# Kernel optimization log

Hardware: AMD Instinct MI355X
Metric: run time of the kernel (lower is better)

## Reference

```python
import jax, jax.numpy as jnp
import numpy as np

B, C, IMG, P, E, H, F, L, NC = 32, 1, 224, 16, 256, 16, 3072, 12, 8
NP_ = (IMG // P) ** 2          # 196 patches
S = NP_ + 1                    # 197 tokens (cls + patches)
HD = E // H                    # 16 head dim
DVL, DVR, DVT = NP_ // 4 + 1, NP_ // 4, NP_ // 4   # 50, 49, 49 -> sum + DVT = 197


def _ln(x, g, b, eps=1e-5):
    m = x.mean(-1, keepdims=True)
    v = ((x - m) ** 2).mean(-1, keepdims=True)
    return (x - m) / jnp.sqrt(v + eps) * g + b


def setup_inputs():
    key = jax.random.key(0)
    ks = iter(jax.random.split(key, 64))
    def w(shape, s=0.02):
        return jax.random.normal(next(ks), shape, jnp.float32) * s
    return dict(
        x=jax.random.normal(next(ks), (B, C, IMG, IMG), jnp.float32),
        W_patch=w((E, C, P, P)), b_patch=jnp.zeros((E,), jnp.float32),
        cls_tok=w((1, 1, E), 1.0), pos_emb=w((1, S, E), 1.0),
        Wkl=w((E, E)), bkl=jnp.zeros((E,), jnp.float32),
        Wvl=w((DVL, E)), bvl=jnp.zeros((DVL,), jnp.float32),
        Wkr=w((E, E)), bkr=jnp.zeros((E,), jnp.float32),
        Wvr=w((DVR, E)), bvr=jnp.zeros((DVR,), jnp.float32),
        Wkt=w((E, E)), bkt=jnp.zeros((E,), jnp.float32),
        Wvt=w((DVT, E)), bvt=jnp.zeros((DVT,), jnp.float32),
        ln1_g=jnp.ones((L, E), jnp.float32), ln1_b=jnp.zeros((L, E), jnp.float32),
        Wqkv=w((L, 3 * E, E)), bqkv=jnp.zeros((L, 3 * E), jnp.float32),
        Wo=w((L, E, E)), bo=jnp.zeros((L, E), jnp.float32),
        ln2_g=jnp.ones((L, E), jnp.float32), ln2_b=jnp.zeros((L, E), jnp.float32),
        W1=w((L, F, E)), b1=jnp.zeros((L, F), jnp.float32),
        W2=w((L, E, F)), b2=jnp.zeros((L, E), jnp.float32),
        lnf_g=jnp.ones((E,), jnp.float32), lnf_b=jnp.zeros((E,), jnp.float32),
        W_head=w((NC, E)), b_head=jnp.zeros((NC,), jnp.float32),
    )


def reference(x, W_patch, b_patch, cls_tok, pos_emb,
              Wkl, bkl, Wvl, bvl, Wkr, bkr, Wvr, bvr, Wkt, bkt, Wvt, bvt,
              ln1_g, ln1_b, Wqkv, bqkv, Wo, bo, ln2_g, ln2_b, W1, b1, W2, b2,
              lnf_g, lnf_b, W_head, b_head):
    Bsz = x.shape[0]
    scale_k = 1.0 / jnp.sqrt(jnp.float32(E))
    # patch embedding: conv with stride == kernel == patch size
    h = jax.lax.conv_general_dilated(x, W_patch, (P, P), 'VALID',
                                     dimension_numbers=('NCHW', 'OIHW', 'NCHW'))
    h = h + b_patch[None, :, None, None]                   # (B, E, 14, 14)
    h = h.reshape(Bsz, E, NP_).transpose(0, 2, 1)          # (B, 196, E)
    h = jnp.concatenate([jnp.broadcast_to(cls_tok, (Bsz, 1, E)), h], 1) + pos_emb

    # linear rotatory attention fusing each sample with its batch neighbors
    def rag(xl, xt, xr):                                   # each (S, E)
        rt = xt.mean(0)                                    # target summary (E,)
        al = jax.nn.softmax((xl @ Wkl.T + bkl) @ rt * scale_k)
        rl = al @ (xl @ Wvl.T + bvl)                       # (DVL,)
        ar = jax.nn.softmax((xr @ Wkr.T + bkr) @ rt * scale_k)
        rr = ar @ (xr @ Wvr.T + bvr)                       # (DVR,)
        kt = xt @ Wkt.T + bkt
        vt = xt @ Wvt.T + bvt
        rtl = jax.nn.softmax(kt @ xl.mean(0) * scale_k) @ vt   # (DVT,)
        rtr = jax.nn.softmax(kt @ xr.mean(0) * scale_k) @ vt   # (DVT,)
        f = jnp.concatenate([rl, rtl, rtr, rr])            # (S,) = 50+49+49+49
        return jnp.outer(f, rt)                            # (S, E)

    mid = jax.vmap(rag)(h[:-2], h[1:-1], h[2:])            # (B-2, S, E) batched (no per-sample loop)
    h = jnp.concatenate([h[:1], mid, h[-1:]], 0)

    # standard pre-LN transformer encoder, scanned over stacked layer params
    def block(carry, p):
        g1, b1n, wqkv, bq, wo, bo_, g2, b2n, w1, bb1, w2, bb2 = p
        xn = _ln(carry, g1, b1n)
        qkv = xn @ wqkv.T + bq                             # (B, S, 3E)
        q, k, v = jnp.split(qkv, 3, axis=-1)
        q = q.reshape(Bsz, S, H, HD)
        k = k.reshape(Bsz, S, H, HD)
        v = v.reshape(Bsz, S, H, HD)
        att = jnp.einsum('bqhd,bkhd->bhqk', q, k) / jnp.sqrt(jnp.float32(HD))
        att = jax.nn.softmax(att, axis=-1)
        o = jnp.einsum('bhqk,bkhd->bqhd', att, v).reshape(Bsz, S, E)
        carry = carry + o @ wo.T + bo_
        xn2 = _ln(carry, g2, b2n)
        ff = jax.nn.gelu(xn2 @ w1.T + bb1, approximate=False) @ w2.T + bb2
        return carry + ff, None

    h, _ = jax.lax.scan(block, h, (ln1_g, ln1_b, Wqkv, bqkv, Wo, bo,
                                   ln2_g, ln2_b, W1, b1, W2, b2))
    cls = _ln(h[:, 0], lnf_g, lnf_b)
    return cls @ W_head.T + b_head
```

## Files before the change

kernel.cpp:

```cpp
#include <hip/hip_runtime.h>
#include <hip/hip_bf16.h>
#include <math.h>

constexpr int Bz  = 32;
constexpr int S   = 197;
constexpr int E   = 256;
constexpr int Hn  = 16;
constexpr int HD  = 16;
constexpr int Fd  = 3072;
constexpr int Ln  = 12;
constexpr int MS  = Bz * S;
constexpr int MP  = 6400;
constexpr int NPAT = 6272;
constexpr int DVL = 50, DVR = 49, DVT = 49;
constexpr size_t WLSTRIDE = 1835008;

typedef __attribute__((ext_vector_type(8))) short short8;
typedef __attribute__((ext_vector_type(4))) short short4v;
typedef __attribute__((ext_vector_type(4))) float f32x4;

__device__ __forceinline__ unsigned short f2bf(float f) {
    unsigned int u = __float_as_uint(f);
    u = (u + 0x7FFFu + ((u >> 16) & 1u)) >> 16;
    return (unsigned short)u;
}

__device__ __forceinline__ void gload_lds16(const void* g, void* l) {
    __builtin_amdgcn_global_load_lds(
        (const __attribute__((address_space(1))) void*)g,
        (__attribute__((address_space(3))) void*)l, 16, 0, 0);
}

__device__ __forceinline__ float wave_reduce(float v, int op) {
    #pragma unroll
    for (int off = 32; off > 0; off >>= 1) {
        float o = __shfl_xor(v, off, 64);
        v = op ? fmaxf(v, o) : v + o;
    }
    return v;
}

__device__ __forceinline__ float block_reduce(float v, float* red4, int op) {
    v = wave_reduce(v, op);
    int w = threadIdx.x >> 6;
    if ((threadIdx.x & 63) == 0) red4[w] = v;
    __syncthreads();
    float r = op ? fmaxf(fmaxf(red4[0], red4[1]), fmaxf(red4[2], red4[3]))
                 : (red4[0] + red4[1] + red4[2] + red4[3]);
    __syncthreads();
    return r;
}

__device__ __forceinline__ float gelu_f(float v) {
    return 0.5f * v * (1.f + erff(v * 0.70710678118654752f));
}

__global__ __launch_bounds__(256) void patchify_kernel(
        const float* __restrict__ x, unsigned short* __restrict__ Ab) {
    int pi = blockIdx.x;
    int b = pi / 196, q = pi % 196;
    int i = q / 14, j = q % 14;
    int e = threadIdx.x, pr = e >> 4, pc = e & 15;
    float v = x[((size_t)(b * 224 + i * 16 + pr)) * 224 + j * 16 + pc];
    Ab[(size_t)pi * 256 + e] = f2bf(v);
}

__global__ __launch_bounds__(256) void cls_pos_kernel(
        const float* __restrict__ cls, const float* __restrict__ pos,
        float* __restrict__ h0) {
    int b = blockIdx.x, e = threadIdx.x;
    h0[(size_t)(b * S) * E + e] = cls[e] + pos[e];
}

__global__ __launch_bounds__(256) void convert_kernel(
        const float* __restrict__ src, unsigned short* __restrict__ dst) {
    int i4 = (blockIdx.x * 256 + threadIdx.x) * 4;
    float4 v = *(const float4*)(src + i4);
    ushort4 o;
    o.x = f2bf(v.x); o.y = f2bf(v.y); o.z = f2bf(v.z); o.w = f2bf(v.w);
    *(ushort4*)(dst + i4) = o;
}

__global__ __launch_bounds__(256) void convert_w_all_kernel(
        const float* __restrict__ wqkv, const float* __restrict__ wo,
        const float* __restrict__ w1, const float* __restrict__ w2,
        unsigned short* __restrict__ out) {
    size_t idx = (size_t)blockIdx.x * 256 + threadIdx.x;
    int l = (int)(idx / 458752);
    int r4 = (int)(idx % 458752) * 4;
    const float* src;
    if (r4 < 196608)       src = wqkv + (size_t)l * 196608 + r4;
    else if (r4 < 262144)  src = wo   + (size_t)l * 65536  + (r4 - 196608);
    else if (r4 < 1048576) src = w1   + (size_t)l * 786432 + (r4 - 262144);
    else                   src = w2   + (size_t)l * 786432 + (r4 - 1048576);
    float4 v = *(const float4*)src;
    ushort4 o;
    o.x = f2bf(v.x); o.y = f2bf(v.y); o.z = f2bf(v.z); o.w = f2bf(v.w);
    *(ushort4*)(out + (size_t)l * WLSTRIDE + r4) = o;
}

__global__ __launch_bounds__(256) void means_kernel(
        const float* __restrict__ h0, float* __restrict__ M) {
    __shared__ float part[4][256];
    int b = blockIdx.x, tid = threadIdx.x, w = tid >> 6, lane = tid & 63;
    float4 a = {0.f, 0.f, 0.f, 0.f};
    for (int t = w; t < S; t += 4) {
        float4 v = *(const float4*)&h0[((size_t)(b * S + t)) * E + lane * 4];
        a.x += v.x; a.y += v.y; a.z += v.z; a.w += v.w;
    }
    *(float4*)&part[w][lane * 4] = a;
    __syncthreads();
    M[b * E + tid] = (part[0][tid] + part[1][tid] + part[2][tid] + part[3][tid])
                     * (1.f / (float)S);
}

__global__ __launch_bounds__(256) void uvec_kernel(
        const float* __restrict__ M,
        const float* __restrict__ Wkl, const float* __restrict__ bkl,
        const float* __restrict__ Wkr, const float* __restrict__ bkr,
        const float* __restrict__ Wkt, const float* __restrict__ bkt,
        float* __restrict__ Ul, float* __restrict__ Ur, float* __restrict__ Ut,
        float* __restrict__ cl, float* __restrict__ cr, float* __restrict__ ct) {
    __shared__ float p0[4][256], p1[4][256], p2[4][256], red4[4];
    int t = blockIdx.x, tid = threadIdx.x, w = tid >> 6, lane = tid & 63;
    const float* mt = M + t * E;
    float4 a0 = {0,0,0,0}, a1 = {0,0,0,0}, a2 = {0,0,0,0};
    for (int i = w * 64; i < w * 64 + 64; i++) {
        float mi = mt[i];
        float4 v0 = *(const float4*)&Wkl[(size_t)i * 256 + lane * 4];
        float4 v1 = *(const float4*)&Wkr[(size_t)i * 256 + lane * 4];
        float4 v2 = *(const float4*)&Wkt[(size_t)i * 256 + lane * 4];
        a0.x += v0.x * mi; a0.y += v0.y * mi; a0.z += v0.z * mi; a0.w += v0.w * mi;
        a1.x += v1.x * mi; a1.y += v1.y * mi; a1.z += v1.z * mi; a1.w += v1.w * mi;
        a2.x += v2.x * mi; a2.y += v2.y * mi; a2.z += v2.z * mi; a2.w += v2.w * mi;
    }
    *(float4*)&p0[w][lane * 4] = a0;
    *(float4*)&p1[w][lane * 4] = a1;
    *(float4*)&p2[w][lane * 4] = a2;
    __syncthreads();
    Ul[t * E + tid] = p0[0][tid] + p0[1][tid] + p0[2][tid] + p0[3][tid];
    Ur[t * E + tid] = p1[0][tid] + p1[1][tid] + p1[2][tid] + p1[3][tid];
    Ut[t * E + tid] = p2[0][tid] + p2[1][tid] + p2[2][tid] + p2[3][tid];
    float me = mt[tid];
    float c0 = block_reduce(bkl[tid] * me, red4, 0);
    float c1 = block_reduce(bkr[tid] * me, red4, 0);
    float c2 = block_reduce(bkt[tid] * me, red4, 0);
    if (tid == 0) { cl[t] = c0; cr[t] = c1; ct[t] = c2; }
}

__global__ __launch_bounds__(256) void rag_score_kernel(
        const float* __restrict__ h0, const float* __restrict__ M,
        const float* __restrict__ Ul, const float* __restrict__ Ur,
        const float* __restrict__ Ut,
        const float* __restrict__ cl, const float* __restrict__ cr,
        const float* __restrict__ ct,
        const float* __restrict__ Wvl, const float* __restrict__ bvl,
        const float* __restrict__ Wvr, const float* __restrict__ bvr,
        const float* __restrict__ Wvt, const float* __restrict__ bvt,
        float* __restrict__ fbuf) {
    int t = blockIdx.x >> 2, br = blockIdx.x & 3;
    const float* xsrc; const float* u; float c;
    const float* Wv; const float* bv; int dv, fo;
    if (br == 0)      { xsrc = h0 + (size_t)t * S * E;       u = Ul + (t+1)*E; c = cl[t+1]; Wv = Wvl; bv = bvl; dv = DVL; fo = 0; }
    else if (br == 1) { xsrc = h0 + (size_t)(t+1) * S * E;   u = Ut + t*E;     c = ct[t];   Wv = Wvt; bv = bvt; dv = DVT; fo = DVL; }
    else if (br == 2) { xsrc = h0 + (size_t)(t+1) * S * E;   u = Ut + (t+2)*E; c = ct[t+2]; Wv = Wvt; bv = bvt; dv = DVT; fo = DVL + DVT; }
    else              { xsrc = h0 + (size_t)(t+2) * S * E;   u = Ur + (t+1)*E; c = cr[t+1]; Wv = Wvr; bv = bvr; dv = DVR; fo = DVL + 2*DVT; }
    __shared__ float us[256], sc[200], xbar[256], part[4][256], red4[4];
    int tid = threadIdx.x, w = tid >> 6, lane = tid & 63;
    us[tid] = u[tid];
    __syncthreads();
    float4 u4 = *(float4*)&us[lane * 4];
    for (int s = w; s < S; s += 4) {
        float4 x4 = *(const float4*)&xsrc[(size_t)s * E + lane * 4];
        float p = x4.x*u4.x + x4.y*u4.y + x4.z*u4.z + x4.w*u4.w;
        p = wave_reduce(p, 0);
        if (lane == 0) sc[s] = (p + c) * 0.0625f;
    }
    __syncthreads();
    float v = (tid < S) ? sc[tid] : -1e30f;
    float mx = block_reduce(v, red4, 1);
    float ex = (tid < S) ? expf(v - mx) : 0.f;
    float dn = block_reduce(ex, red4, 0);
    if (tid < S) sc[tid] = ex / dn;
    __syncthreads();
    float4 pa = {0.f, 0.f, 0.f, 0.f};
    for (int s = w; s < S; s += 4) {
        float a = sc[s];
        float4 x4 = *(const float4*)&xsrc[(size_t)s * E + lane * 4];
        pa.x += a * x4.x; pa.y += a * x4.y; pa.z += a * x4.z; pa.w += a * x4.w;
    }
    *(float4*)&part[w][lane * 4] = pa;
    __syncthreads();
    xbar[tid] = part[0][tid] + part[1][tid] + part[2][tid] + part[3][tid];
    __syncthreads();
    float4 xb4 = *(float4*)&xbar[lane * 4];
    for (int d = w; d < dv; d += 4) {
        float4 w4 = *(const float4*)&Wv[(size_t)d * E + lane * 4];
        float p = w4.x*xb4.x + w4.y*xb4.y + w4.z*xb4.z + w4.w*xb4.w;
        p = wave_reduce(p, 0);
        if (lane == 0) fbuf[t * 256 + fo + d] = p + bv[d];
    }
}

__global__ __launch_bounds__(256) void rag_outer_kernel(
        const float* __restrict__ fbuf, const float* __restrict__ M,
        float* __restrict__ h1) {
    int bid = blockIdx.x;
    int t = bid / S, s = bid % S;
    float f = fbuf[t * 256 + s];
    int e = threadIdx.x;
    h1[((size_t)((t + 1) * S + s)) * E + e] = f * M[(t + 1) * E + e];
}

__global__ __launch_bounds__(256) void copy_edges(const float* __restrict__ h0,
                                                  float* __restrict__ h1) {
    int i = blockIdx.x * 256 + threadIdx.x;
    int n = S * E;
    if (i < n) h1[i] = h0[i];
    else if (i < 2 * n) {
        int j = i - n;
        size_t o = (size_t)31 * S * E + j;
        h1[o] = h0[o];
    }
}

__global__ __launch_bounds__(256) void ln_kernel(const float* __restrict__ in,
                                                 unsigned short* __restrict__ out,
                                                 const float* __restrict__ g,
                                                 const float* __restrict__ b) {
    int w = threadIdx.x >> 6, lane = threadIdx.x & 63;
    int tok = blockIdx.x * 4 + w;
    const float* row = in + (size_t)tok * E;
    float4 v = *(const float4*)&row[lane * 4];
    float mean = wave_reduce(v.x + v.y + v.z + v.w, 0) * (1.f / 256.f);
    float dx = v.x - mean, dy = v.y - mean, dz = v.z - mean, dw = v.w - mean;
    float var = wave_reduce(dx*dx + dy*dy + dz*dz + dw*dw, 0) * (1.f / 256.f);
    float inv = rsqrtf(var + 1e-5f);
    float4 gg = *(const float4*)&g[lane * 4];
    float4 bb = *(const float4*)&b[lane * 4];
    ushort4 o;
    o.x = f2bf(dx * inv * gg.x + bb.x);
    o.y = f2bf(dy * inv * gg.y + bb.y);
    o.z = f2bf(dz * inv * gg.z + bb.z);
    o.w = f2bf(dw * inv * gg.w + bb.w);
    *(ushort4*)&out[(size_t)tok * E + lane * 4] = o;
}

template <int MODE>
__global__ __launch_bounds__(256) void gemm_s64(
        const unsigned short* __restrict__ A, int lda,
        const unsigned short* __restrict__ W, int ldw,
        const float* __restrict__ bias,
        void* __restrict__ Cv, int ldc, int K, int MT, int NT,
        const float* __restrict__ pos) {
    constexpr bool SWAP = (MODE == 4);
    __shared__ unsigned short As[2 * 64 * 64];
    __shared__ unsigned short Bs[2 * 64 * 64];
    const int id = blockIdx.x;
    const int mt = (id & 7) + 8 * (id / (8 * NT));
    const int nt = (id >> 3) % NT;
    if (mt >= MT) return;
    const int m0 = mt * 64, n0 = nt * 64;
    const int tid = threadIdx.x, wave = tid >> 6, lane = tid & 63;
    const int lr = lane & 15, kg = lane >> 4;
    const int srow = wave * 16 + (lane >> 3);
    const int scol = ((lane & 7) ^ (lane >> 3)) * 8;
    auto stage = [&](int bb, int k0) {
        #pragma unroll
        for (int q = 0; q < 2; q++) {
            gload_lds16(&A[(size_t)(m0 + srow + q * 8) * lda + k0 + scol],
                        &As[bb * 4096 + (wave * 16 + q * 8) * 64]);
            gload_lds16(&W[(size_t)(n0 + srow + q * 8) * ldw + k0 + scol],
                        &Bs[bb * 4096 + (wave * 16 + q * 8) * 64]);
        }
    };
    const int nIter = K >> 6;
    stage(0, 0);
    f32x4 acc[4] = {};
    for (int i = 0; i < nIter; i++) {
        __syncthreads();
        if (i + 1 < nIter) stage((i + 1) & 1, (i + 1) * 64);
        const int bb = i & 1;
        #pragma unroll
        for (int h = 0; h < 2; h++) {
            const int sw = ((h * 4 + kg) ^ (lr & 7)) * 8;
            short8 af = *(short8*)&As[bb * 4096 + (wave * 16 + lr) * 64 + sw];
            #pragma unroll
            for (int j = 0; j < 4; j++) {
                short8 bf = *(short8*)&Bs[bb * 4096 + (j * 16 + lr) * 64 + sw];
                if (SWAP)
                    acc[j] = __builtin_amdgcn_mfma_f32_16x16x32_bf16(bf, af, acc[j], 0, 0, 0);
                else
                    acc[j] = __builtin_amdgcn_mfma_f32_16x16x32_bf16(af, bf, acc[j], 0, 0, 0);
            }
        }
    }
    if (SWAP) {
        __syncthreads();
        unsigned short* T = As + wave * 1152;
        #pragma unroll
        for (int j = 0; j < 4; j++) {
            int nb = n0 + j * 16 + kg * 4;
            float4 b4 = *(const float4*)&bias[nb];
            ushort4 pk;
            pk.x = f2bf(acc[j][0] + b4.x);
            pk.y = f2bf(acc[j][1] + b4.y);
            pk.z = f2bf(acc[j][2] + b4.z);
            pk.w = f2bf(acc[j][3] + b4.w);
            *(ushort4*)&T[lr * 72 + j * 16 + kg * 4] = pk;
        }
        int rrow = lane >> 3, cg = (lane & 7) * 8;
        #pragma unroll
        for (int g = 0; g < 2; g++) {
            int row = g * 8 + rrow;
            short8 val = *(short8*)&T[row * 72 + cg];
            int m = m0 + wave * 16 + row;
            *(short8*)&((unsigned short*)Cv)[(size_t)m * ldc + n0 + cg] = val;
        }
    } else {
        #pragma unroll
        for (int j = 0; j < 4; j++) {
            int n = n0 + j * 16 + lr;
            float bv = bias ? bias[n] : 0.f;
            #pragma unroll
            for (int r = 0; r < 4; r++) {
                int m = m0 + wave * 16 + kg * 4 + r;
                float v = acc[j][r] + bv;
                if (MODE == 1) ((float*)Cv)[(size_t)m * ldc + n] += v;
                if (MODE == 3) {
                    int b = m / 196, s = m - b * 196 + 1;
                    ((float*)Cv)[((size_t)(b * S + s)) * E + n] = v + pos[(size_t)s * E + n];
                }
            }
        }
    }
}

template <int MODE>
__global__ __launch_bounds__(256) void gemm_s128(
        const unsigned short* __restrict__ A, int lda,
        const unsigned short* __restrict__ W, int ldw,
        const float* __restrict__ bias,
        void* __restrict__ Cv, int ldc, int K, int MT, int NT) {
    __shared__ unsigned short As[2 * 128 * 64];
    __shared__ unsigned short Bs[2 * 128 * 64];
    const int id = blockIdx.x;
    const int mt = (id & 7) + 8 * (id / (8 * NT));
    const int nt = (id >> 3) % NT;
    if (mt >= MT) return;
    const int m0 = mt * 128, n0 = nt * 128;
    const int tid = threadIdx.x, wave = tid >> 6, lane = tid & 63;
    const int wm = (wave >> 1) * 64, wn = (wave & 1) * 64;
    const int lr = lane & 15, kg = lane >> 4;
    const int srow = wave * 32 + (lane >> 3);
    const int scol = ((lane & 7) ^ (lane >> 3)) * 8;
    auto stage = [&](int bb, int k0) {
        #pragma unroll
        for (int q = 0; q < 4; q++) {
            gload_lds16(&A[(size_t)(m0 + srow + q * 8) * lda + k0 + scol],
                        &As[bb * 8192 + (wave * 4 + q) * 512]);
            gload_lds16(&W[(size_t)(n0 + srow + q * 8) * ldw + k0 + scol],
                        &Bs[bb * 8192 + (wave * 4 + q) * 512]);
        }
    };
    const int nIter = K >> 6;
    stage(0, 0);
    f32x4 acc[4][4] = {};
    for (int i = 0; i < nIter; i++) {
        __syncthreads();
        if (i + 1 < nIter) stage((i + 1) & 1, (i + 1) * 64);
        const int bb = i & 1;
        #pragma unroll
        for (int h = 0; h < 2; h++) {
            const int sw = ((h * 4 + kg) ^ (lr & 7)) * 8;
            short8 af[4], bfr[4];
            #pragma unroll
            for (int i2 = 0; i2 < 4; i2++) af[i2]  = *(short8*)&As[bb * 8192 + (wm + i2 * 16 + lr) * 64 + sw];
            #pragma unroll
            for (int j = 0; j < 4; j++) bfr[j] = *(short8*)&Bs[bb * 8192 + (wn + j * 16 + lr) * 64 + sw];
            #pragma unroll
            for (int i2 = 0; i2 < 4; i2++)
                #pragma unroll
                for (int j = 0; j < 4; j++)
                    acc[i2][j] = __builtin_amdgcn_mfma_f32_16x16x32_bf16(bfr[j], af[i2], acc[i2][j], 0, 0, 0);
        }
    }
    __syncthreads();
    unsigned short* T = As + wave * 2304;
    #pragma unroll
    for (int half = 0; half < 2; half++) {
        #pragma unroll
        for (int ii = 0; ii < 2; ii++) {
            int i = half * 2 + ii;
            #pragma unroll
            for (int j = 0; j < 4; j++) {
                int nb = n0 + wn + j * 16 + kg * 4;
                float4 b4 = *(const float4*)&bias[nb];
                ushort4 pk;
                pk.x = f2bf(gelu_f(acc[i][j][0] + b4.x));
                pk.y = f2bf(gelu_f(acc[i][j][1] + b4.y));
                pk.z = f2bf(gelu_f(acc[i][j][2] + b4.z));
                pk.w = f2bf(gelu_f(acc[i][j][3] + b4.w));
                *(ushort4*)&T[(ii * 16 + lr) * 72 + j * 16 + kg * 4] = pk;
            }
        }
        int rrow = lane >> 3, cg = (lane & 7) * 8;
        #pragma unroll
        for (int g = 0; g < 4; g++) {
            int row = g * 8 + rrow;
            short8 val = *(short8*)&T[row * 72 + cg];
            int m = m0 + wm + half * 32 + row;
            *(short8*)&((unsigned short*)Cv)[(size_t)m * ldc + n0 + wn + cg] = val;
        }
        if (half == 0) __syncthreads();
    }
}

static inline int sg(int MT, int NT) { return ((MT + 7) / 8) * 8 * NT; }

__global__ __launch_bounds__(256) void attn_kernel(
        const unsigned short* __restrict__ qkv, unsigned short* __restrict__ o) {
    int b = blockIdx.x >> 4, hh = blockIdx.x & 15;
    __shared__ unsigned short Qs[208][32];
    __shared__ unsigned short Ks[208][32];
    __shared__ unsigned short Vt[16][224];
    __shared__ unsigned short Ps[4][16][224];
    int tid = threadIdx.x, wave = tid >> 6, lane = tid & 63;
    int lr = lane & 15, kg = lane >> 4;
    short8 z8 = {};
    if (tid < 208) {
        if (tid < 197) {
            size_t row = (size_t)(b * S + tid) * 768 + hh * 16;
            *(short8*)&Qs[tid][0] = *(const short8*)&qkv[row];
            *(short8*)&Qs[tid][8] = *(const short8*)&qkv[row + 8];
            *(short8*)&Ks[tid][0] = *(const short8*)&qkv[row + 256];
            *(short8*)&Ks[tid][8] = *(const short8*)&qkv[row + 264];
            union { short8 v8[2]; unsigned short u[16]; } vv;
            vv.v8[0] = *(const short8*)&qkv[row + 512];
            vv.v8[1] = *(const short8*)&qkv[row + 520];
            #pragma unroll
            for (int d = 0; d < 16; d++) Vt[d][tid] = vv.u[d];
        } else {
            *(short8*)&Qs[tid][0] = z8; *(short8*)&Qs[tid][8] = z8;
            *(short8*)&Ks[tid][0] = z8; *(short8*)&Ks[tid][8] = z8;
            #pragma unroll
            for (int d = 0; d < 16; d++) Vt[d][tid] = 0;
        }
        *(short8*)&Qs[tid][16] = z8; *(short8*)&Qs[tid][24] = z8;
        *(short8*)&Ks[tid][16] = z8; *(short8*)&Ks[tid][24] = z8;
    } else if (tid < 224) {
        #pragma unroll
        for (int d = 0; d < 16; d++) Vt[d][tid] = 0;
    }
    {
        short4v z4 = {};
        *(short4v*)&Ps[wave][lane >> 2][208 + (lane & 3) * 4] = z4;
    }
    __syncthreads();
    const f32x4 zf = {0.f, 0.f, 0.f, 0.f};
    for (int it = wave; it < 13; it += 4) {
        short8 qa = *(short8*)&Qs[it * 16 + lr][kg * 8];
        f32x4 sc[13];
        #pragma unroll
        for (int j = 0; j < 13; j++) {
            short8 kb = *(short8*)&Ks[j * 16 + lr][kg * 8];
            sc[j] = __builtin_amdgcn_mfma_f32_16x16x32_bf16(qa, kb, zf, 0, 0, 0);
        }
        float m[4] = {-1e30f, -1e30f, -1e30f, -1e30f};
        #pragma unroll
        for (int j = 0; j < 13; j++) {
            if (j * 16 + lr < 197) {
                #pragma unroll
                for (int r = 0; r < 4; r++) m[r] = fmaxf(m[r], sc[j][r]);
            }
        }
        #pragma unroll
        for (int off = 1; off < 16; off <<= 1)
            #pragma unroll
            for (int r = 0; r < 4; r++) m[r] = fmaxf(m[r], __shfl_xor(m[r], off, 64));
        float l[4] = {0.f, 0.f, 0.f, 0.f};
        #pragma unroll
        for (int j = 0; j < 13; j++) {
            bool valid = (j * 16 + lr) < 197;
            #pragma unroll
            for (int r = 0; r < 4; r++) {
                float p = valid ? __expf((sc[j][r] - m[r]) * 0.25f) : 0.f;
                l[r] += p;
                Ps[wave][kg * 4 + r][j * 16 + lr] = f2bf(p);
            }
        }
        #pragma unroll
        for (int off = 1; off < 16; off <<= 1)
            #pragma unroll
            for (int r = 0; r < 4; r++) l[r] += __shfl_xor(l[r], off, 64);
        f32x4 oa = zf;
        #pragma unroll
        for (int k0 = 0; k0 < 224; k0 += 32) {
            short8 pa = *(short8*)&Ps[wave][lr][k0 + kg * 8];
            short8 vb = *(short8*)&Vt[lr][k0 + kg * 8];
            oa = __builtin_amdgcn_mfma_f32_16x16x32_bf16(pa, vb, oa, 0, 0, 0);
        }
        #pragma unroll
        for (int r = 0; r < 4; r++) {
            int q = it * 16 + kg * 4 + r;
            if (q < 197)
                o[((size_t)(b * S + q)) * 256 + hh * 16 + lr] = f2bf(oa[r] / l[r]);
        }
    }
}

__global__ __launch_bounds__(256) void head_kernel(
        const float* __restrict__ h, const float* __restrict__ g,
        const float* __restrict__ bb, const float* __restrict__ Wh,
        const float* __restrict__ bh, float* __restrict__ out) {
    __shared__ float red4[4];
    __shared__ float xs[256];
    int b = blockIdx.x, e = threadIdx.x;
    float v = h[((size_t)(b * S)) * E + e];
    float mean = block_reduce(v, red4, 0) * (1.f / 256.f);
    float d = v - mean;
    float var = block_reduce(d * d, red4, 0) * (1.f / 256.f);
    float xn = d * rsqrtf(var + 1e-5f) * g[e] + bb[e];
    xs[e] = xn;
    __syncthreads();
    for (int n = 0; n < 8; n++) {
        float s = block_reduce(xs[e] * Wh[(size_t)n * 256 + e], red4, 0);
        if (e == 0) out[b * 8 + n] = s + bh[n];
    }
}

extern "C" void kernel_launch(void* const* d_in, const int* in_sizes, int n_in,
                              void* d_out, int out_size, void* d_ws, size_t ws_size,
                              hipStream_t stream) {
    const float* x      = (const float*)d_in[0];
    const float* W_patch= (const float*)d_in[1];
    const float* b_patch= (const float*)d_in[2];
    const float* cls_tok= (const float*)d_in[3];
    const float* pos_emb= (const float*)d_in[4];
    const float* Wkl = (const float*)d_in[5];   const float* bkl = (const float*)d_in[6];
    const float* Wvl = (const float*)d_in[7];   const float* bvl = (const float*)d_in[8];
    const float* Wkr = (const float*)d_in[9];   const float* bkr = (const float*)d_in[10];
    const float* Wvr = (const float*)d_in[11];  const float* bvr = (const float*)d_in[12];
    const float* Wkt = (const float*)d_in[13];  const float* bkt = (const float*)d_in[14];
    const float* Wvt = (const float*)d_in[15];  const float* bvt = (const float*)d_in[16];
    const float* ln1_g = (const float*)d_in[17]; const float* ln1_b = (const float*)d_in[18];
    const float* Wqkv  = (const float*)d_in[19]; const float* bqkv  = (const float*)d_in[20];
    const float* Wo    = (const float*)d_in[21]; const float* bo    = (const float*)d_in[22];
    const float* ln2_g = (const float*)d_in[23]; const float* ln2_b = (const float*)d_in[24];
    const float* W1 = (const float*)d_in[25];   const float* b1 = (const float*)d_in[26];
    const float* W2 = (const float*)d_in[27];   const float* b2 = (const float*)d_in[28];
    const float* lnf_g = (const float*)d_in[29]; const float* lnf_b = (const float*)d_in[30];
    const float* W_head = (const float*)d_in[31]; const float* b_head = (const float*)d_in[32];

    char* p = (char*)d_ws;
    float* h0 = (float*)p;                    p += (size_t)MP * 256 * 4;
    float* h1 = (float*)p;                    p += (size_t)MP * 256 * 4;
    unsigned short* qkb = (unsigned short*)p; p += (size_t)MP * 768 * 2;
    unsigned short* xnb = (unsigned short*)p; p += (size_t)MP * 256 * 2;
    unsigned short* ob  = (unsigned short*)p; p += (size_t)MP * 256 * 2;
    unsigned short* ff  = (unsigned short*)p; p += (size_t)MP * 3072 * 2;
    unsigned short* wpb = (unsigned short*)p; p += (size_t)65536 * 2;
    float* ragws = (float*)p;                 p += (size_t)40960 * 4;
    unsigned short* wall = (unsigned short*)p;
    float* M    = ragws;
    float* Ul   = ragws + 8192;
    float* Ur   = ragws + 2 * 8192;
    float* Ut   = ragws + 3 * 8192;
    float* cl   = ragws + 4 * 8192;
    float* cr   = cl + 32;
    float* ct   = cl + 64;
    float* fbuf = cl + 96;

    convert_w_all_kernel<<<21504, 256, 0, stream>>>(Wqkv, Wo, W1, W2, wall);

    convert_kernel<<<64, 256, 0, stream>>>(W_patch, wpb);
    patchify_kernel<<<NPAT, 256, 0, stream>>>(x, xnb);
    cls_pos_kernel<<<Bz, 256, 0, stream>>>(cls_tok, pos_emb, h0);
    gemm_s64<3><<<sg(98, 4), 256, 0, stream>>>(
        xnb, 256, wpb, 256, b_patch, h0, 256, 256, 98, 4, pos_emb);

    means_kernel<<<Bz, 256, 0, stream>>>(h0, M);
    uvec_kernel<<<Bz, 256, 0, stream>>>(M, Wkl, bkl, Wkr, bkr, Wkt, bkt,
                                        Ul, Ur, Ut, cl, cr, ct);
    rag_score_kernel<<<(Bz - 2) * 4, 256, 0, stream>>>(
        h0, M, Ul, Ur, Ut, cl, cr, ct, Wvl, bvl, Wvr, bvr, Wvt, bvt, fbuf);
    rag_outer_kernel<<<(Bz - 2) * S, 256, 0, stream>>>(fbuf, M, h1);
    copy_edges<<<(2 * S * E + 255) / 256, 256, 0, stream>>>(h0, h1);

    for (int l = 0; l < Ln; l++) {
        const unsigned short* wqkv_b = wall + (size_t)l * WLSTRIDE;
        const unsigned short* wo_b   = wqkv_b + 196608;
        const unsigned short* w1_b   = wqkv_b + 262144;
        const unsigned short* w2_b   = wqkv_b + 1048576;
        ln_kernel<<<MS / 4, 256, 0, stream>>>(h1, xnb, ln1_g + l * E, ln1_b + l * E);
        gemm_s64<4><<<sg(100, 12), 256, 0, stream>>>(
            xnb, 256, wqkv_b, 256, bqkv + l * 768, qkb, 768, 256, 100, 12, nullptr);
        attn_kernel<<<Bz * Hn, 256, 0, stream>>>(qkb, ob);
        gemm_s64<1><<<sg(100, 4), 256, 0, stream>>>(
            ob, 256, wo_b, 256, bo + l * 256, h1, 256, 256, 100, 4, nullptr);
        ln_kernel<<<MS / 4, 256, 0, stream>>>(h1, xnb, ln2_g + l * E, ln2_b + l * E);
        gemm_s128<2><<<sg(50, 24), 256, 0, stream>>>(
            xnb, 256, w1_b, 256, b1 + l * Fd, ff, 3072, 256, 50, 24);
        gemm_s64<1><<<sg(100, 4), 256, 0, stream>>>(
            ff, 3072, w2_b, 3072, b2 + l * 256, h1, 256, 3072, 100, 4, nullptr);
    }
    head_kernel<<<Bz, 256, 0, stream>>>(h1, lnf_g, lnf_b, W_head, b_head, (float*)d_out);
}
```

Baseline: 1.637 ms.

## Specialize FFN1 GEMM: preload full A tile, stream W from global, polynomial GELU

The FFN1 GEMM becomes a specialized kernel with K fixed at 256. It loads the whole 128x256 A tile into LDS once with a single barrier, and streams weight fragments straight from global memory into registers, double-buffered across the eight k-steps. This removes the per-iteration barriers and the LDS staging for B. It also replaces erff in GELU with the Abramowitz-Stegun polynomial plus __expf, which cuts epilogue cost but adds an approximation error of about 1e-7 in erf.

Result: slower. 1.772 ms (+8.3%).

```diff
diff --git a/kernel.cpp b/kernel.cpp
--- a/kernel.cpp
+++ b/kernel.cpp
@@ -52,7 +52,14 @@
 }
 
 __device__ __forceinline__ float gelu_f(float v) {
-    return 0.5f * v * (1.f + erff(v * 0.70710678118654752f));
+    float x  = v * 0.70710678118654752f;
+    float ax = fabsf(x);
+    float t  = 1.0f / fmaf(0.3275911f, ax, 1.0f);
+    float p  = t * fmaf(t, fmaf(t, fmaf(t, fmaf(t, 1.061405429f, -1.453152027f),
+                                        1.421413741f), -0.284496736f), 0.254829592f);
+    float er = 1.0f - p * __expf(-x * x);
+    er = copysignf(er, x);
+    return 0.5f * v * (1.0f + er);
 }
 
 __global__ __launch_bounds__(256) void patchify_kernel(
@@ -336,14 +343,14 @@
     }
 }
 
-template <int MODE>
-__global__ __launch_bounds__(256) void gemm_s128(
-        const unsigned short* __restrict__ A, int lda,
-        const unsigned short* __restrict__ W, int ldw,
+__global__ __launch_bounds__(256) void gemm_ffn1(
+        const unsigned short* __restrict__ A,
+        const unsigned short* __restrict__ W,
         const float* __restrict__ bias,
-        void* __restrict__ Cv, int ldc, int K, int MT, int NT) {
-    __shared__ unsigned short As[2 * 128 * 64];
-    __shared__ unsigned short Bs[2 * 128 * 64];
+        unsigned short* __restrict__ Cv,
+        int MT, int NT) {
+    constexpr int LDA = 256, LDW = 256, LDC = 3072;
+    __shared__ unsigned short As[4 * 128 * 64];
     const int id = blockIdx.x;
     const int mt = (id & 7) + 8 * (id / (8 * NT));
     const int nt = (id >> 3) % NT;
@@ -354,35 +361,39 @@
     const int lr = lane & 15, kg = lane >> 4;
     const int srow = wave * 32 + (lane >> 3);
     const int scol = ((lane & 7) ^ (lane >> 3)) * 8;
-    auto stage = [&](int bb, int k0) {
-        #pragma unroll
-        for (int q = 0; q < 4; q++) {
-            gload_lds16(&A[(size_t)(m0 + srow + q * 8) * lda + k0 + scol],
-                        &As[bb * 8192 + (wave * 4 + q) * 512]);
-            gload_lds16(&W[(size_t)(n0 + srow + q * 8) * ldw + k0 + scol],
-                        &Bs[bb * 8192 + (wave * 4 + q) * 512]);
-        }
+    #pragma unroll
+    for (int c = 0; c < 4; c++)
+        #pragma unroll
+        for (int q = 0; q < 4; q++)
+            gload_lds16(&A[(size_t)(m0 + srow + q * 8) * LDA + c * 64 + scol],
+                        &As[c * 8192 + (wave * 4 + q) * 512]);
+    const unsigned short* Wrow[4];
+    #pragma unroll
+    for (int j = 0; j < 4; j++)
+        Wrow[j] = W + (size_t)(n0 + wn + j * 16 + lr) * LDW + kg * 8;
+    f32x4 acc[4][4] = {};
+    short8 bfA[4], bfB[4];
+    auto loadB = [&](short8 (&dst)[4], int s) {
+        #pragma unroll
+        for (int j = 0; j < 4; j++)
+            dst[j] = *(const short8*)(Wrow[j] + s * 32);
     };
-    const int nIter = K >> 6;
-    stage(0, 0);
-    f32x4 acc[4][4] = {};
-    for (int i = 0; i < nIter; i++) {
-        __syncthreads();
-        if (i + 1 < nIter) stage((i + 1) & 1, (i + 1) * 64);
-        const int bb = i & 1;
-        #pragma unroll
-        for (int h = 0; h < 2; h++) {
-            const int sw = ((h * 4 + kg) ^ (lr & 7)) * 8;
-            short8 af[4], bfr[4];
-            #pragma unroll
-            for (int i2 = 0; i2 < 4; i2++) af[i2]  = *(short8*)&As[bb * 8192 + (wm + i2 * 16 + lr) * 64 + sw];
-            #pragma unroll
-            for (int j = 0; j < 4; j++) bfr[j] = *(short8*)&Bs[bb * 8192 + (wn + j * 16 + lr) * 64 + sw];
-            #pragma unroll
-            for (int i2 = 0; i2 < 4; i2++)
-                #pragma unroll
-                for (int j = 0; j < 4; j++)
-                    acc[i2][j] = __builtin_amdgcn_mfma_f32_16x16x32_bf16(bfr[j], af[i2], acc[i2][j], 0, 0, 0);
+    loadB(bfA, 0);
+    __syncthreads();
+    #pragma unroll
+    for (int s = 0; s < 8; s++) {
+        const int c = s >> 1, h = s & 1;
+        const int sw = ((h * 4 + kg) ^ (lr & 7)) * 8;
+        short8 (&cur)[4] = (s & 1) ? bfB : bfA;
+        short8 (&nxt)[4] = (s & 1) ? bfA : bfB;
+        if (s < 7) loadB(nxt, s + 1);
+        #pragma unroll
+        for (int i2 = 0; i2 < 4; i2++) {
+            short8 af = *(short8*)&As[c * 8192 + (wm + i2 * 16 + lr) * 64 + sw];
+            #pragma unroll
+            for (int j = 0; j < 4; j++)
+                acc[i2][j] = __builtin_amdgcn_mfma_f32_16x16x32_bf16(
+                        cur[j], af, acc[i2][j], 0, 0, 0);
         }
     }
     __syncthreads();
@@ -410,7 +421,7 @@
             int row = g * 8 + rrow;
             short8 val = *(short8*)&T[row * 72 + cg];
             int m = m0 + wm + half * 32 + row;
-            *(short8*)&((unsigned short*)Cv)[(size_t)m * ldc + n0 + wn + cg] = val;
+            *(short8*)&Cv[(size_t)m * LDC + n0 + wn + cg] = val;
         }
         if (half == 0) __syncthreads();
     }
@@ -599,8 +610,8 @@
         gemm_s64<1><<<sg(100, 4), 256, 0, stream>>>(
             ob, 256, wo_b, 256, bo + l * 256, h1, 256, 256, 100, 4, nullptr);
         ln_kernel<<<MS / 4, 256, 0, stream>>>(h1, xnb, ln2_g + l * E, ln2_b + l * E);
-        gemm_s128<2><<<sg(50, 24), 256, 0, stream>>>(
-            xnb, 256, w1_b, 256, b1 + l * Fd, ff, 3072, 256, 50, 24);
+        gemm_ffn1<<<sg(50, 24), 256, 0, stream>>>(
+            xnb, w1_b, b1 + l * Fd, ff, 50, 24);
         gemm_s64<1><<<sg(100, 4), 256, 0, stream>>>(
             ff, 3072, w2_b, 3072, b2 + l * 256, h1, 256, 3072, 100, 4, nullptr);
     }
```
